# Performance work log

Measured on AMD Instinct MI355X. Metric: run time of the kernel, lower is better.

## Reference

```python
import jax, jax.numpy as jnp
import numpy as np

N_HEAD = 16


def setup_inputs() -> dict:
    key = jax.random.key(0)
    ks = jax.random.split(key, 9)
    b, s, d = 4, 2048, 1024
    scale = 1.0 / np.sqrt(d)
    return {
        "x": jax.random.normal(ks[0], (b, s, d), dtype=jnp.float32),
        "Wq": jax.random.normal(ks[1], (d, d), dtype=jnp.float32) * scale,
        "bq": jax.random.normal(ks[2], (d,), dtype=jnp.float32) * 0.01,
        "Wk": jax.random.normal(ks[3], (d, d), dtype=jnp.float32) * scale,
        "bk": jax.random.normal(ks[4], (d,), dtype=jnp.float32) * 0.01,
        "Wv": jax.random.normal(ks[5], (d, d), dtype=jnp.float32) * scale,
        "bv": jax.random.normal(ks[6], (d,), dtype=jnp.float32) * 0.01,
        "Wo": jax.random.normal(ks[7], (d, d), dtype=jnp.float32) * scale,
        "bo": jax.random.normal(ks[8], (d,), dtype=jnp.float32) * 0.01,
        "mask": 1,
    }


def reference(x, Wq, bq, Wk, bk, Wv, bv, Wo, bo, mask):
    b, s, d = x.shape
    h = N_HEAD
    dh = d // h
    # projections -> [b, h, s, dh]
    def proj(W, bias):
        return (x @ W + bias).reshape(b, s, h, dh).transpose(0, 2, 1, 3)

    Q = proj(Wq, bq)
    K = proj(Wk, bk)
    V = proj(Wv, bv)

    # full S x S scores (module materializes them explicitly)
    scores = jnp.einsum('bhqd,bhkd->bhqk', Q, K)
    if mask:
        causal = jnp.triu(jnp.ones((s, s), dtype=bool), k=1)
        scores = jnp.where(causal, -jnp.inf, scores)
    scores = scores / jnp.sqrt(jnp.asarray(dh, dtype=scores.dtype))
    attn = jax.nn.softmax(scores, axis=-1)
    out = jnp.einsum('bhqk,bhkd->bhqd', attn, V)  # [b, h, s, dh]
    out = out.transpose(0, 2, 1, 3).reshape(b, s, d)
    return out @ Wo + bo
```

## Files before the change

kernel.cpp:

```cpp
#include <hip/hip_runtime.h>

typedef unsigned short u16;
typedef unsigned int u32;
typedef __bf16 bf16x8 __attribute__((ext_vector_type(8)));
typedef float f32x4 __attribute__((ext_vector_type(4)));

#define BATCH 4
#define SLEN 2048
#define DMODEL 1024
#define NHEAD 16
#define DHEAD 64
#define MROWS (BATCH * SLEN)

__device__ __forceinline__ u16 f32_to_bf16(float f) {
  u32 u = __float_as_uint(f);
  u32 r = (u + 0x7FFFu + ((u >> 16) & 1u)) >> 16;
  return (u16)r;
}
__device__ __forceinline__ u32 pack_bf16x2(float a, float b) {
  return (u32)f32_to_bf16(a) | ((u32)f32_to_bf16(b) << 16);
}

__device__ __forceinline__ u32 pack_trunc(float lo, float hi) {
#if __has_builtin(__builtin_amdgcn_perm)
  return __builtin_amdgcn_perm(__float_as_uint(hi), __float_as_uint(lo), 0x07060302u);
#else
  return (__float_as_uint(hi) & 0xFFFF0000u) | (__float_as_uint(lo) >> 16);
#endif
}
__device__ __forceinline__ u32 pack_round(float lo, float hi) {
  u32 ul = __float_as_uint(lo) + 0x8000u;
  u32 uh = __float_as_uint(hi) + 0x8000u;
#if __has_builtin(__builtin_amdgcn_perm)
  return __builtin_amdgcn_perm(uh, ul, 0x07060302u);
#else
  return (uh & 0xFFFF0000u) | (ul >> 16);
#endif
}

#if __has_builtin(__builtin_amdgcn_exp2f)
#define EXP2(x) __builtin_amdgcn_exp2f(x)
#else
#define EXP2(x) exp2f(x)
#endif

typedef const __attribute__((address_space(1))) void* gas_cv;
typedef __attribute__((address_space(3))) void* las_v;
__device__ __forceinline__ void async16(const u16* g, u16* l) {
  __builtin_amdgcn_global_load_lds((gas_cv)g, (las_v)l, 16, 0, 0);
}


__global__ void convert_x_kernel(const float* __restrict__ x, u16* __restrict__ xb) {
  size_t i = ((size_t)blockIdx.x * 256 + threadIdx.x) * 8;
  float4 v0 = *(const float4*)(x + i);
  float4 v1 = *(const float4*)(x + i + 4);
  uint4 o;
  o.x = pack_bf16x2(v0.x, v0.y);
  o.y = pack_bf16x2(v0.z, v0.w);
  o.z = pack_bf16x2(v1.x, v1.y);
  o.w = pack_bf16x2(v1.z, v1.w);
  *(uint4*)(xb + i) = o;
}

__global__ void transpose_w_kernel(const float* __restrict__ Wq, const float* __restrict__ Wk,
                                   const float* __restrict__ Wv, const float* __restrict__ Wo,
                                   u16* __restrict__ wqkvt, u16* __restrict__ wot) {
  __shared__ float tile[32][33];
  int z = blockIdx.z;
  const float* src = (z == 0) ? Wq : (z == 1) ? Wk : (z == 2) ? Wv : Wo;
  u16* dst = (z < 3) ? (wqkvt + (size_t)z * DMODEL * DMODEL) : wot;
  int c0 = blockIdx.x * 32, r0 = blockIdx.y * 32;
  int tx = threadIdx.x & 31, ty = threadIdx.x >> 5;
#pragma unroll
  for (int i = 0; i < 4; ++i)
    tile[ty + 8 * i][tx] = src[(size_t)(r0 + ty + 8 * i) * DMODEL + c0 + tx];
  __syncthreads();
#pragma unroll
  for (int i = 0; i < 4; ++i)
    dst[(size_t)(c0 + ty + 8 * i) * DMODEL + r0 + tx] = f32_to_bf16(tile[tx][ty + 8 * i]);
}

__global__ void concat_bias_kernel(const float* __restrict__ bq, const float* __restrict__ bk,
                                   const float* __restrict__ bv, float* __restrict__ bqkv) {
  int i = blockIdx.x * 256 + threadIdx.x;
  float v = (i < 1024) ? bq[i] : (i < 2048) ? bk[i - 1024] : bv[i - 2048];
  bqkv[i] = v;
}

__global__ void transpose_v_kernel(const u16* __restrict__ qkv, u16* __restrict__ vt) {
  __shared__ u16 tile[32][33];
  const int bh = blockIdx.z;
  const int b = bh >> 4, h = bh & 15;
  const int s0 = blockIdx.x * 32, d0 = blockIdx.y * 32;
  const int tx = threadIdx.x & 31, ty = threadIdx.x >> 5;
#pragma unroll
  for (int i = 0; i < 4; ++i)
    tile[ty + 8 * i][tx] =
        qkv[(size_t)(b * SLEN + s0 + ty + 8 * i) * (3 * DMODEL) + 2 * DMODEL + h * DHEAD + d0 + tx];
  __syncthreads();
#pragma unroll
  for (int i = 0; i < 4; ++i)
    vt[(size_t)(bh * DHEAD + d0 + ty + 8 * i) * SLEN + s0 + tx] = tile[tx][ty + 8 * i];
}

template <int OUT_BF16>
__global__ __launch_bounds__(256) void gemm_bt_kernel(const u16* __restrict__ A,
                                                      const u16* __restrict__ Bt,
                                                      const float* __restrict__ bias,
                                                      void* __restrict__ Cout,
                                                      int M, int N, int K) {
  __shared__ u16 sA[128 * 32];
  __shared__ u16 sB[128 * 32];
  const int tid = threadIdx.x;
  const int wv = tid >> 6, lane = tid & 63;
  const int wr = wv >> 1, wc = wv & 1;
  const int col = lane & 15, quad = lane >> 4;
  const int m0 = blockIdx.x * 128;
  const int n0 = blockIdx.y * 128;

  f32x4 acc[4][4] = {};

  const int lr = tid >> 2;
  const int ls = tid & 3;
  const size_t a_base = (size_t)(m0 + lr) * K + ls * 8;
  const size_t b_base = (size_t)(n0 + lr) * K + ls * 8;
  u16* ldsA0 = sA + ((tid >> 6) << 9);
  u16* ldsA1 = ldsA0 + 2048;
  u16* ldsB0 = sB + ((tid >> 6) << 9);
  u16* ldsB1 = ldsB0 + 2048;

  for (int k0 = 0; k0 < K; k0 += 32) {
    async16(A + a_base + k0, ldsA0);
    async16(A + a_base + (size_t)64 * K + k0, ldsA1);
    async16(Bt + b_base + k0, ldsB0);
    async16(Bt + b_base + (size_t)64 * K + k0, ldsB1);
    __syncthreads();
    bf16x8 af[4], bfr[4];
#pragma unroll
    for (int i = 0; i < 4; ++i)
      af[i] = *(const bf16x8*)(sA + (wr * 64 + i * 16 + col) * 32 + quad * 8);
#pragma unroll
    for (int j = 0; j < 4; ++j)
      bfr[j] = *(const bf16x8*)(sB + (wc * 64 + j * 16 + col) * 32 + quad * 8);
#pragma unroll
    for (int i = 0; i < 4; ++i)
#pragma unroll
      for (int j = 0; j < 4; ++j)
        acc[i][j] = __builtin_amdgcn_mfma_f32_16x16x32_bf16(af[i], bfr[j], acc[i][j], 0, 0, 0);
    __syncthreads();
  }

#pragma unroll
  for (int i = 0; i < 4; ++i) {
#pragma unroll
    for (int j = 0; j < 4; ++j) {
      int n = n0 + wc * 64 + j * 16 + col;
      float bia = bias[n];
#pragma unroll
      for (int r = 0; r < 4; ++r) {
        int m = m0 + wr * 64 + i * 16 + quad * 4 + r;
        float v = acc[i][j][r] + bia;
        if (OUT_BF16)
          ((u16*)Cout)[(size_t)m * N + n] = f32_to_bf16(v);
        else
          ((float*)Cout)[(size_t)m * N + n] = v;
      }
    }
  }
}

__global__ __launch_bounds__(256, 2) void attn_kernel(const u16* __restrict__ qkv,
                                                      const u16* __restrict__ vt,
                                                      u16* __restrict__ out) {
  const int bh = blockIdx.y;
  const int b = bh >> 4, h = bh & 15;
  const int tid = threadIdx.x;
  const int wv = tid >> 6, lane = tid & 63;
  const int col = lane & 15, quad = lane >> 4;
  const int bx = blockIdx.x;
  const int sfirst = bx * 4 + wv;

  __shared__ u16 sK[2][64 * 64];
  __shared__ u16 sV[2][64 * 64];
  __shared__ u16 sP[4][32 * 72];
  u16* mysP = sP[wv];

  const u16* kbase = qkv + ((size_t)(b * SLEN)) * (3 * DMODEL) + DMODEL + h * DHEAD;
  const u16* vbase = vt + ((size_t)bh * DHEAD) * SLEN;
  const float scl2 = 0.125f * 1.44269504088896f;

  const int lrow = lane >> 3;
  const int sga = (lane & 7) ^ lrow;
  const int r0a = wv * 16, r0b = wv * 16 + 8;
  const int swz = ((quad ) ^ (col & 7)) * 8;

  for (int half = 0; half < 2; ++half) {
    const int s2 = half ? (63 - sfirst) : sfirst;
    const int qbase = s2 * 32;
    const int nt_own = s2 / 2 + 1;
    const int nt_max = half ? (32 - 2 * bx) : (2 * bx + 2);

    const u16* qrow = qkv + ((size_t)(b * SLEN + qbase + col)) * (3 * DMODEL) + h * DHEAD;
    bf16x8 aQ[2][2];
#pragma unroll
    for (int i = 0; i < 2; ++i)
#pragma unroll
      for (int ks = 0; ks < 2; ++ks)
        aQ[i][ks] = *(const bf16x8*)(qrow + (size_t)i * 16 * (3 * DMODEL) + ks * 32 + quad * 8);

    f32x4 accO[2][4] = {};
    float m2[2] = {-1e30f, -1e30f}, l_i[2] = {0.0f, 0.0f};

    async16(kbase + (size_t)(r0a + lrow) * (3 * DMODEL) + sga * 8, sK[0] + r0a * 64);
    async16(kbase + (size_t)(r0b + lrow) * (3 * DMODEL) + sga * 8, sK[0] + r0b * 64);
    async16(vbase + (size_t)(r0a + lrow) * SLEN + sga * 8, sV[0] + r0a * 64);
    async16(vbase + (size_t)(r0b + lrow) * SLEN + sga * 8, sV[0] + r0b * 64);
    __syncthreads();

    for (int t = 0; t < nt_max; ++t) {
      const int kv0 = t * 64;
      const int cur = t & 1, nxt = cur ^ 1;

      if (t + 1 < nt_max) {
        const int kvn = kv0 + 64;
        async16(kbase + (size_t)(kvn + r0a + lrow) * (3 * DMODEL) + sga * 8, sK[nxt] + r0a * 64);
        async16(kbase + (size_t)(kvn + r0b + lrow) * (3 * DMODEL) + sga * 8, sK[nxt] + r0b * 64);
        async16(vbase + (size_t)(r0a + lrow) * SLEN + kvn + sga * 8, sV[nxt] + r0a * 64);
        async16(vbase + (size_t)(r0b + lrow) * SLEN + kvn + sga * 8, sV[nxt] + r0b * 64);
      }

      if (t < nt_own) {
        const u16* sKc = sK[cur];
        const u16* sVc = sV[cur];
        bf16x8 bK[2][4], bV[2][4];
#pragma unroll
        for (int ks = 0; ks < 2; ++ks) {
          const int sl = (((ks * 4 + quad) ^ (col & 7)) * 8);
#pragma unroll
          for (int cb = 0; cb < 4; ++cb)
            bK[ks][cb] = *(const bf16x8*)(sKc + (cb * 16 + col) * 64 + sl);
#pragma unroll
          for (int j = 0; j < 4; ++j)
            bV[ks][j] = *(const bf16x8*)(sVc + (j * 16 + col) * 64 + sl);
        }

        f32x4 accST[2][4] = {};
#pragma unroll
        for (int ks = 0; ks < 2; ++ks)
#pragma unroll
          for (int cb = 0; cb < 4; ++cb)
#pragma unroll
            for (int i = 0; i < 2; ++i)
              accST[i][cb] = __builtin_amdgcn_mfma_f32_16x16x32_bf16(bK[ks][cb], aQ[i][ks],
                                                                    accST[i][cb], 0, 0, 0);

        if (t == nt_own - 1) {
#pragma unroll
          for (int i = 0; i < 2; ++i) {
            int q = qbase + i * 16 + col;
#pragma unroll
            for (int cb = 0; cb < 4; ++cb) {
              int kvb = kv0 + cb * 16 + quad * 4;
#pragma unroll
              for (int r = 0; r < 4; ++r)
                if (kvb + r > q) accST[i][cb][r] = -1e30f;
            }
          }
        }

        float rmax[2], mnew[2], alpha[2], rsum[2];
#pragma unroll
        for (int i = 0; i < 2; ++i) {
          float m = accST[i][0][0];
#pragma unroll
          for (int cb = 0; cb < 4; ++cb)
#pragma unroll
            for (int r = 0; r < 4; ++r) m = fmaxf(m, accST[i][cb][r]);
          rmax[i] = m;
        }
#pragma unroll
        for (int i = 0; i < 2; ++i) {
          rmax[i] = fmaxf(rmax[i], __shfl_xor(rmax[i], 16));
          rmax[i] = fmaxf(rmax[i], __shfl_xor(rmax[i], 32));
          mnew[i] = fmaxf(m2[i], rmax[i] * scl2);
          alpha[i] = EXP2(m2[i] - mnew[i]);
          m2[i] = mnew[i];
        }
#pragma unroll
        for (int i = 0; i < 2; ++i) {
          float sacc = 0.0f;
#pragma unroll
          for (int cb = 0; cb < 4; ++cb)
#pragma unroll
            for (int r = 0; r < 4; ++r) {
              float p = EXP2(__builtin_fmaf(accST[i][cb][r], scl2, -mnew[i]));
              accST[i][cb][r] = p;
              sacc += p;
            }
          rsum[i] = sacc;
        }
#pragma unroll
        for (int i = 0; i < 2; ++i) {
          rsum[i] += __shfl_xor(rsum[i], 16);
          rsum[i] += __shfl_xor(rsum[i], 32);
          l_i[i] = l_i[i] * alpha[i] + rsum[i];
        }
#pragma unroll
        for (int i = 0; i < 2; ++i)
#pragma unroll
          for (int j = 0; j < 4; ++j)
#pragma unroll
            for (int r = 0; r < 4; ++r) accO[i][j][r] *= alpha[i];

#pragma unroll
        for (int i = 0; i < 2; ++i)
#pragma unroll
          for (int cb = 0; cb < 4; ++cb) {
            uint2 pk;
            pk.x = pack_trunc(accST[i][cb][0], accST[i][cb][1]);
            pk.y = pack_trunc(accST[i][cb][2], accST[i][cb][3]);
            *(uint2*)(mysP + (i * 16 + col) * 72 + cb * 16 + quad * 4) = pk;
          }
        bf16x8 aP[2][2];
#pragma unroll
        for (int i = 0; i < 2; ++i)
#pragma unroll
          for (int ks = 0; ks < 2; ++ks)
            aP[i][ks] = *(const bf16x8*)(mysP + (i * 16 + col) * 72 + ks * 32 + quad * 8);

#pragma unroll
        for (int ks = 0; ks < 2; ++ks)
#pragma unroll
          for (int j = 0; j < 4; ++j)
#pragma unroll
            for (int i = 0; i < 2; ++i)
              accO[i][j] = __builtin_amdgcn_mfma_f32_16x16x32_bf16(bV[ks][j], aP[i][ks],
                                                                  accO[i][j], 0, 0, 0);
      }

      __syncthreads();
    }

#pragma unroll
    for (int i = 0; i < 2; ++i) {
      float rl = 1.0f / l_i[i];
      size_t rowoff = ((size_t)(b * SLEN + qbase + i * 16 + col)) * DMODEL + h * DHEAD;
#pragma unroll
      for (int j = 0; j < 4; ++j) {
        uint2 pk;
        pk.x = pack_round(accO[i][j][0] * rl, accO[i][j][1] * rl);
        pk.y = pack_round(accO[i][j][2] * rl, accO[i][j][3] * rl);
        *(uint2*)(out + rowoff + j * 16 + quad * 4) = pk;
      }
    }
  }
}


extern "C" void kernel_launch(void* const* d_in, const int* in_sizes, int n_in,
                              void* d_out, int out_size, void* d_ws, size_t ws_size,
                              hipStream_t stream) {
  const float* x = (const float*)d_in[0];
  const float* Wq = (const float*)d_in[1];
  const float* bq = (const float*)d_in[2];
  const float* Wk = (const float*)d_in[3];
  const float* bk = (const float*)d_in[4];
  const float* Wv = (const float*)d_in[5];
  const float* bv = (const float*)d_in[6];
  const float* Wo = (const float*)d_in[7];
  const float* bo = (const float*)d_in[8];

  char* ws = (char*)d_ws;
  u16* xb = (u16*)ws;
  u16* wqkvt = (u16*)(ws + ((size_t)16 << 20));
  u16* wot = (u16*)(ws + ((size_t)22 << 20));
  u16* qkv = (u16*)(ws + ((size_t)24 << 20));
  u16* attnO = (u16*)(ws + ((size_t)72 << 20));
  float* bqkv = (float*)(ws + ((size_t)88 << 20));
  u16* vtp = xb;

  convert_x_kernel<<<4096, 256, 0, stream>>>(x, xb);
  transpose_w_kernel<<<dim3(32, 32, 4), 256, 0, stream>>>(Wq, Wk, Wv, Wo, wqkvt, wot);
  concat_bias_kernel<<<12, 256, 0, stream>>>(bq, bk, bv, bqkv);
  gemm_bt_kernel<1><<<dim3(64, 24), 256, 0, stream>>>(xb, wqkvt, bqkv, (void*)qkv,
                                                      MROWS, 3 * DMODEL, DMODEL);
  transpose_v_kernel<<<dim3(64, 2, 64), 256, 0, stream>>>(qkv, vtp);
  attn_kernel<<<dim3(8, BATCH * NHEAD), 256, 0, stream>>>(qkv, vtp, attnO);
  gemm_bt_kernel<0><<<dim3(64, 8), 256, 0, stream>>>(attnO, wot, bo, d_out,
                                                     MROWS, DMODEL, DMODEL);
}
```

Before: 291.5 us.

## Shrink attention per-wave query tile to 16 rows and double grid

Each wave now handles 16 query rows instead of 32, and the grid doubles to 16 blocks per head. All four waves in a block now share the same number of KV tiles, so the per-wave causal skip branch goes away. The P scratch buffer is made smaller with an XOR-swizzled layout, and launch bounds are raised to allow 4 blocks per CU. The aim is more parallelism and occupancy with less idle wave time, at the cost of each K/V tile load being reused by fewer query rows, which means more LDS and global traffic per FLOP.

```diff
diff --git a/kernel.cpp b/kernel.cpp
--- a/kernel.cpp
+++ b/kernel.cpp
@@ -170,7 +170,7 @@
   }
 }
 
-__global__ __launch_bounds__(256, 2) void attn_kernel(const u16* __restrict__ qkv,
+__global__ __launch_bounds__(256, 4) void attn_kernel(const u16* __restrict__ qkv,
                                                       const u16* __restrict__ vt,
                                                       u16* __restrict__ out) {
   const int bh = blockIdx.y;
@@ -183,7 +183,7 @@
 
   __shared__ u16 sK[2][64 * 64];
   __shared__ u16 sV[2][64 * 64];
-  __shared__ u16 sP[4][32 * 72];
+  __shared__ u16 sP[4][16 * 64];
   u16* mysP = sP[wv];
 
   const u16* kbase = qkv + ((size_t)(b * SLEN)) * (3 * DMODEL) + DMODEL + h * DHEAD;
@@ -193,24 +193,20 @@
   const int lrow = lane >> 3;
   const int sga = (lane & 7) ^ lrow;
   const int r0a = wv * 16, r0b = wv * 16 + 8;
-  const int swz = ((quad ) ^ (col & 7)) * 8;
 
   for (int half = 0; half < 2; ++half) {
-    const int s2 = half ? (63 - sfirst) : sfirst;
-    const int qbase = s2 * 32;
-    const int nt_own = s2 / 2 + 1;
-    const int nt_max = half ? (32 - 2 * bx) : (2 * bx + 2);
+    const int s2 = half ? (127 - sfirst) : sfirst;
+    const int qbase = s2 * 16;
+    const int nt = half ? (32 - bx) : (bx + 1);
 
     const u16* qrow = qkv + ((size_t)(b * SLEN + qbase + col)) * (3 * DMODEL) + h * DHEAD;
-    bf16x8 aQ[2][2];
-#pragma unroll
-    for (int i = 0; i < 2; ++i)
-#pragma unroll
-      for (int ks = 0; ks < 2; ++ks)
-        aQ[i][ks] = *(const bf16x8*)(qrow + (size_t)i * 16 * (3 * DMODEL) + ks * 32 + quad * 8);
-
-    f32x4 accO[2][4] = {};
-    float m2[2] = {-1e30f, -1e30f}, l_i[2] = {0.0f, 0.0f};
+    bf16x8 aQ[2];
+#pragma unroll
+    for (int ks = 0; ks < 2; ++ks)
+      aQ[ks] = *(const bf16x8*)(qrow + ks * 32 + quad * 8);
+
+    f32x4 accO[4] = {};
+    float m2 = -1e30f, l_i = 0.0f;
 
     async16(kbase + (size_t)(r0a + lrow) * (3 * DMODEL) + sga * 8, sK[0] + r0a * 64);
     async16(kbase + (size_t)(r0b + lrow) * (3 * DMODEL) + sga * 8, sK[0] + r0b * 64);
@@ -218,11 +214,11 @@
     async16(vbase + (size_t)(r0b + lrow) * SLEN + sga * 8, sV[0] + r0b * 64);
     __syncthreads();
 
-    for (int t = 0; t < nt_max; ++t) {
+    for (int t = 0; t < nt; ++t) {
       const int kv0 = t * 64;
       const int cur = t & 1, nxt = cur ^ 1;
 
-      if (t + 1 < nt_max) {
+      if (t + 1 < nt) {
         const int kvn = kv0 + 64;
         async16(kbase + (size_t)(kvn + r0a + lrow) * (3 * DMODEL) + sga * 8, sK[nxt] + r0a * 64);
         async16(kbase + (size_t)(kvn + r0b + lrow) * (3 * DMODEL) + sga * 8, sK[nxt] + r0b * 64);
@@ -230,127 +226,97 @@
         async16(vbase + (size_t)(r0b + lrow) * SLEN + kvn + sga * 8, sV[nxt] + r0b * 64);
       }
 
-      if (t < nt_own) {
-        const u16* sKc = sK[cur];
-        const u16* sVc = sV[cur];
-        bf16x8 bK[2][4], bV[2][4];
-#pragma unroll
-        for (int ks = 0; ks < 2; ++ks) {
-          const int sl = (((ks * 4 + quad) ^ (col & 7)) * 8);
-#pragma unroll
-          for (int cb = 0; cb < 4; ++cb)
-            bK[ks][cb] = *(const bf16x8*)(sKc + (cb * 16 + col) * 64 + sl);
-#pragma unroll
-          for (int j = 0; j < 4; ++j)
-            bV[ks][j] = *(const bf16x8*)(sVc + (j * 16 + col) * 64 + sl);
+      const u16* sKc = sK[cur];
+      const u16* sVc = sV[cur];
+      bf16x8 bK[2][4], bV[2][4];
+#pragma unroll
+      for (int ks = 0; ks < 2; ++ks) {
+        const int sl = (((ks * 4 + quad) ^ (col & 7)) * 8);
+#pragma unroll
+        for (int cb = 0; cb < 4; ++cb)
+          bK[ks][cb] = *(const bf16x8*)(sKc + (cb * 16 + col) * 64 + sl);
+#pragma unroll
+        for (int j = 0; j < 4; ++j)
+          bV[ks][j] = *(const bf16x8*)(sVc + (j * 16 + col) * 64 + sl);
+      }
+
+      f32x4 accST[4] = {};
+#pragma unroll
+      for (int ks = 0; ks < 2; ++ks)
+#pragma unroll
+        for (int cb = 0; cb < 4; ++cb)
+          accST[cb] = __builtin_amdgcn_mfma_f32_16x16x32_bf16(bK[ks][cb], aQ[ks],
+                                                              accST[cb], 0, 0, 0);
+
+      if (t == nt - 1) {
+        int q = qbase + col;
+#pragma unroll
+        for (int cb = 0; cb < 4; ++cb) {
+          int kvb = kv0 + cb * 16 + quad * 4;
+#pragma unroll
+          for (int r = 0; r < 4; ++r)
+            if (kvb + r > q) accST[cb][r] = -1e30f;
         }
-
-        f32x4 accST[2][4] = {};
-#pragma unroll
-        for (int ks = 0; ks < 2; ++ks)
-#pragma unroll
-          for (int cb = 0; cb < 4; ++cb)
-#pragma unroll
-            for (int i = 0; i < 2; ++i)
-              accST[i][cb] = __builtin_amdgcn_mfma_f32_16x16x32_bf16(bK[ks][cb], aQ[i][ks],
-                                                                    accST[i][cb], 0, 0, 0);
-
-        if (t == nt_own - 1) {
-#pragma unroll
-          for (int i = 0; i < 2; ++i) {
-            int q = qbase + i * 16 + col;
-#pragma unroll
-            for (int cb = 0; cb < 4; ++cb) {
-              int kvb = kv0 + cb * 16 + quad * 4;
-#pragma unroll
-              for (int r = 0; r < 4; ++r)
-                if (kvb + r > q) accST[i][cb][r] = -1e30f;
-            }
-          }
+      }
+
+      float rmax = accST[0][0];
+#pragma unroll
+      for (int cb = 0; cb < 4; ++cb)
+#pragma unroll
+        for (int r = 0; r < 4; ++r) rmax = fmaxf(rmax, accST[cb][r]);
+      rmax = fmaxf(rmax, __shfl_xor(rmax, 16));
+      rmax = fmaxf(rmax, __shfl_xor(rmax, 32));
+      float mnew = fmaxf(m2, rmax * scl2);
+      float alpha = EXP2(m2 - mnew);
+      m2 = mnew;
+      float sacc = 0.0f;
+#pragma unroll
+      for (int cb = 0; cb < 4; ++cb)
+#pragma unroll
+        for (int r = 0; r < 4; ++r) {
+          float p = EXP2(__builtin_fmaf(accST[cb][r], scl2, -mnew));
+          accST[cb][r] = p;
+          sacc += p;
         }
-
-        float rmax[2], mnew[2], alpha[2], rsum[2];
-#pragma unroll
-        for (int i = 0; i < 2; ++i) {
-          float m = accST[i][0][0];
-#pragma unroll
-          for (int cb = 0; cb < 4; ++cb)
-#pragma unroll
-            for (int r = 0; r < 4; ++r) m = fmaxf(m, accST[i][cb][r]);
-          rmax[i] = m;
-        }
-#pragma unroll
-        for (int i = 0; i < 2; ++i) {
-          rmax[i] = fmaxf(rmax[i], __shfl_xor(rmax[i], 16));
-          rmax[i] = fmaxf(rmax[i], __shfl_xor(rmax[i], 32));
-          mnew[i] = fmaxf(m2[i], rmax[i] * scl2);
-          alpha[i] = EXP2(m2[i] - mnew[i]);
-          m2[i] = mnew[i];
-        }
-#pragma unroll
-        for (int i = 0; i < 2; ++i) {
-          float sacc = 0.0f;
-#pragma unroll
-          for (int cb = 0; cb < 4; ++cb)
-#pragma unroll
-            for (int r = 0; r < 4; ++r) {
-              float p = EXP2(__builtin_fmaf(accST[i][cb][r], scl2, -mnew[i]));
-              accST[i][cb][r] = p;
-              sacc += p;
-            }
-          rsum[i] = sacc;
-        }
-#pragma unroll
-        for (int i = 0; i < 2; ++i) {
-          rsum[i] += __shfl_xor(rsum[i], 16);
-          rsum[i] += __shfl_xor(rsum[i], 32);
-          l_i[i] = l_i[i] * alpha[i] + rsum[i];
-        }
-#pragma unroll
-        for (int i = 0; i < 2; ++i)
-#pragma unroll
-          for (int j = 0; j < 4; ++j)
-#pragma unroll
-            for (int r = 0; r < 4; ++r) accO[i][j][r] *= alpha[i];
-
-#pragma unroll
-        for (int i = 0; i < 2; ++i)
-#pragma unroll
-          for (int cb = 0; cb < 4; ++cb) {
-            uint2 pk;
-            pk.x = pack_trunc(accST[i][cb][0], accST[i][cb][1]);
-            pk.y = pack_trunc(accST[i][cb][2], accST[i][cb][3]);
-            *(uint2*)(mysP + (i * 16 + col) * 72 + cb * 16 + quad * 4) = pk;
-          }
-        bf16x8 aP[2][2];
-#pragma unroll
-        for (int i = 0; i < 2; ++i)
-#pragma unroll
-          for (int ks = 0; ks < 2; ++ks)
-            aP[i][ks] = *(const bf16x8*)(mysP + (i * 16 + col) * 72 + ks * 32 + quad * 8);
-
-#pragma unroll
-        for (int ks = 0; ks < 2; ++ks)
-#pragma unroll
-          for (int j = 0; j < 4; ++j)
-#pragma unroll
-            for (int i = 0; i < 2; ++i)
-              accO[i][j] = __builtin_amdgcn_mfma_f32_16x16x32_bf16(bV[ks][j], aP[i][ks],
-                                                                  accO[i][j], 0, 0, 0);
-      }
+      sacc += __shfl_xor(sacc, 16);
+      sacc += __shfl_xor(sacc, 32);
+      l_i = l_i * alpha + sacc;
+#pragma unroll
+      for (int j = 0; j < 4; ++j)
+#pragma unroll
+        for (int r = 0; r < 4; ++r) accO[j][r] *= alpha;
+
+#pragma unroll
+      for (int cb = 0; cb < 4; ++cb) {
+        uint2 pk;
+        pk.x = pack_trunc(accST[cb][0], accST[cb][1]);
+        pk.y = pack_trunc(accST[cb][2], accST[cb][3]);
+        *(uint2*)(mysP + col * 64 + (((cb * 2 + (quad >> 1)) ^ (col & 7)) << 3) +
+                  ((quad & 1) << 2)) = pk;
+      }
+      bf16x8 aP[2];
+#pragma unroll
+      for (int ks = 0; ks < 2; ++ks)
+        aP[ks] = *(const bf16x8*)(mysP + col * 64 + (((ks * 4 + quad) ^ (col & 7)) << 3));
+
+#pragma unroll
+      for (int ks = 0; ks < 2; ++ks)
+#pragma unroll
+        for (int j = 0; j < 4; ++j)
+          accO[j] = __builtin_amdgcn_mfma_f32_16x16x32_bf16(bV[ks][j], aP[ks],
+                                                            accO[j], 0, 0, 0);
 
       __syncthreads();
     }
 
-#pragma unroll
-    for (int i = 0; i < 2; ++i) {
-      float rl = 1.0f / l_i[i];
-      size_t rowoff = ((size_t)(b * SLEN + qbase + i * 16 + col)) * DMODEL + h * DHEAD;
+    {
+      float rl = 1.0f / l_i;
+      size_t rowoff = ((size_t)(b * SLEN + qbase + col)) * DMODEL + h * DHEAD;
 #pragma unroll
       for (int j = 0; j < 4; ++j) {
         uint2 pk;
-        pk.x = pack_round(accO[i][j][0] * rl, accO[i][j][1] * rl);
-        pk.y = pack_round(accO[i][j][2] * rl, accO[i][j][3] * rl);
+        pk.x = pack_round(accO[j][0] * rl, accO[j][1] * rl);
+        pk.y = pack_round(accO[j][2] * rl, accO[j][3] * rl);
         *(uint2*)(out + rowoff + j * 16 + quad * 4) = pk;
       }
     }
@@ -386,7 +352,7 @@
   gemm_bt_kernel<1><<<dim3(64, 24), 256, 0, stream>>>(xb, wqkvt, bqkv, (void*)qkv,
                                                       MROWS, 3 * DMODEL, DMODEL);
   transpose_v_kernel<<<dim3(64, 2, 64), 256, 0, stream>>>(qkv, vtp);
-  attn_kernel<<<dim3(8, BATCH * NHEAD), 256, 0, stream>>>(qkv, vtp, attnO);
+  attn_kernel<<<dim3(16, BATCH * NHEAD), 256, 0, stream>>>(qkv, vtp, attnO);
   gemm_bt_kernel<0><<<dim3(64, 8), 256, 0, stream>>>(attnO, wot, bo, d_out,
                                                      MROWS, DMODEL, DMODEL);
 }
```

New measurement: 299.2 us. +2.7%, slower.
